# Performance work log

Measured on AMD Instinct MI355X. Metric: run time of the kernel, lower is better.

Reference implementation:

```python
import jax, jax.numpy as jnp
import numpy as np

N = 100000      # nodes
E = 1600000     # edges
IN_DIM = 128    # node_feat_dim
HID = 64        # hidden_dim
K = 3           # Chebyshev order
LAMBDA_MAX = 2.0  # PyG ChebConv default for 'sym' normalization


def setup_inputs():
    key = jax.random.key(0)
    ks = jax.random.split(key, 11)
    x = jax.random.normal(ks[0], (N, IN_DIM), jnp.float32)
    edge_index = jax.random.randint(ks[1], (2, E), 0, N)
    edge_weight = jax.random.uniform(ks[2], (E,), jnp.float32)
    h = jax.random.normal(ks[3], (N, HID), jnp.float32)
    c = jax.random.normal(ks[4], (N, HID), jnp.float32)
    s_in = 1.0 / np.sqrt(IN_DIM)
    s_h = 1.0 / np.sqrt(HID)
    # stacked gate params, order: [input, forget, cell(candidate), output]
    Wx = jax.random.uniform(ks[5], (4, IN_DIM, HID), jnp.float32, -s_in, s_in)
    bg = jax.random.uniform(ks[6], (4, HID), jnp.float32, -s_h, s_h)
    theta = jax.random.uniform(ks[7], (4, K, HID, HID), jnp.float32, -s_h, s_h)
    conv_b = jax.random.uniform(ks[8], (4, HID), jnp.float32, -s_h, s_h)
    Wl = jax.random.uniform(ks[9], (HID, HID), jnp.float32, -s_h, s_h)
    bl = jax.random.uniform(ks[10], (HID,), jnp.float32, -s_h, s_h)
    return dict(x=x, edge_index=edge_index, edge_weight=edge_weight, h=h, c=c,
                Wx=Wx, bg=bg, theta=theta, conv_b=conv_b, Wl=Wl, bl=bl)


def _make_lhat_mm(edge_index, edge_weight, num_nodes, lambda_max):
    # Builds z -> L_hat @ z  with  L_hat = (2/lambda_max) * (I - D^-1/2 A D^-1/2) - I
    src, dst = edge_index[0], edge_index[1]
    w = jnp.where(src == dst, 0.0, edge_weight)  # remove_self_loops
    deg = jax.ops.segment_sum(w, src, num_segments=num_nodes)
    deg_safe = jnp.where(deg > 0, deg, 1.0)
    dinv = jnp.where(deg > 0, jax.lax.rsqrt(deg_safe), 0.0)  # inf -> 0 as in PyG
    lap_w = (2.0 / lambda_max) * (-dinv[src] * w * dinv[dst])  # scaled off-diagonal
    diag = 2.0 / lambda_max - 1.0                              # scaled diag (0 at lmax=2)
    def lhat_mm(z):
        msg = lap_w[:, None] * z[src]                       # [E, HID] gather
        agg = jax.ops.segment_sum(msg, dst, num_segments=num_nodes)
        return agg + diag * z
    return lhat_mm


def reference(x, edge_index, edge_weight, h, c, Wx, bg, theta, conv_b, Wl, bl):
    lhat_mm = _make_lhat_mm(edge_index, edge_weight, x.shape[0], LAMBDA_MAX)
    # Chebyshev basis T_k(L_hat) h ; identical across the 4 gate ChebConvs, so compute once.
    Tx = [h, lhat_mm(h)]
    for _ in range(2, K):
        Tx.append(2.0 * lhat_mm(Tx[-1]) - Tx[-2])
    Tx = jnp.stack(Tx)                                      # [K, N, HID]
    conv = jnp.einsum('knh,gkho->gno', Tx, theta) + conv_b[:, None, :]
    lin = jnp.einsum('nf,gfo->gno', x, Wx) + bg[:, None, :]
    pre = lin + conv                                        # [4, N, HID]
    i = jax.nn.sigmoid(pre[0])
    f = jax.nn.sigmoid(pre[1])
    t = jnp.tanh(pre[2])
    o = jax.nn.sigmoid(pre[3])
    c0 = f * c + i * t
    h0 = o * jnp.tanh(c0)
    out = jax.nn.relu(h0) @ Wl + bl                         # trailing relu + Linear
    return (out, h0, c0)
```

## Files before the change

kernel.cpp:

```cpp
#include <hip/hip_runtime.h>
#include <hip/hip_bf16.h>

#define NN 100000
#define NE 1600000
#define INDIM 128
#define HID 64
#define BSH 9
#define NBUCK 196

typedef __hip_bfloat16 bf16;
typedef unsigned short ushort;
typedef unsigned int uint;
typedef __attribute__((ext_vector_type(8))) short short8;
typedef __attribute__((ext_vector_type(4))) float floatx4;

__device__ __forceinline__ float b2f(bf16 v) { return __bfloat162float(v); }
__device__ __forceinline__ float b2f_raw(ushort u) { return __uint_as_float(((uint)u) << 16); }
__device__ __forceinline__ ushort f2bu(float v) {
    bf16 t = __float2bfloat16(v);
    return *reinterpret_cast<ushort*>(&t);
}
__device__ __forceinline__ float ldin(const void* p, int i, int f32) {
    return f32 ? ((const float*)p)[i] : b2f(((const bf16*)p)[i]);
}
__device__ __forceinline__ float sigmoidf(float x) { return 1.f / (1.f + __expf(-x)); }
__device__ __forceinline__ float tanh_fast(float x) {
    float e = __expf(2.f * x);
    return 1.f - 2.f / (e + 1.f);
}
__device__ __forceinline__ uint4 packf8(const float* f) {
    uint4 u;
    u.x = f2bu(f[0]) | ((uint)f2bu(f[1]) << 16);
    u.y = f2bu(f[2]) | ((uint)f2bu(f[3]) << 16);
    u.z = f2bu(f[4]) | ((uint)f2bu(f[5]) << 16);
    u.w = f2bu(f[6]) | ((uint)f2bu(f[7]) << 16);
    return u;
}
__device__ __forceinline__ uint4 ld8_bf16(const void* p, int off, int f32) {
    if (!f32) return *(const uint4*)((const ushort*)p + off);
    const float* q = (const float*)p + off;
    float4 a = *(const float4*)q, b = *(const float4*)(q + 4);
    float f[8] = {a.x, a.y, a.z, a.w, b.x, b.y, b.z, b.w};
    return packf8(f);
}
__device__ __forceinline__ void ld4w(const void* ew, int e0, int f32, float* w) {
    if (f32) {
        float4 v = *(const float4*)((const float*)ew + e0);
        w[0] = v.x; w[1] = v.y; w[2] = v.z; w[3] = v.w;
    } else {
        uint2 v = *(const uint2*)((const ushort*)ew + e0);
        w[0] = b2f_raw((ushort)(v.x & 0xffff)); w[1] = b2f_raw((ushort)(v.x >> 16));
        w[2] = b2f_raw((ushort)(v.y & 0xffff)); w[3] = b2f_raw((ushort)(v.y >> 16));
    }
}

__global__ void k_sniff(const void* __restrict__ x, int* __restrict__ flag) {
    __shared__ int cnt;
    if (threadIdx.x == 0) cnt = 0;
    __syncthreads();
    const bf16* p = (const bf16*)x;
    int bad = 0;
    for (int i = threadIdx.x; i < 8192; i += 256) {
        float v = b2f(p[i]);
        if (!(fabsf(v) < 1e6f)) bad++;
    }
    atomicAdd(&cnt, bad);
    __syncthreads();
    if (threadIdx.x == 0) flag[0] = (cnt > 32) ? 1 : 0;
}

__global__ __launch_bounds__(256)
void k_count(const int* __restrict__ ei, int* __restrict__ gcntD,
             int* __restrict__ gcntS) {
    __shared__ int hD[NBUCK], hS[NBUCK];
    for (int i = threadIdx.x; i < NBUCK; i += 256) { hD[i] = 0; hS[i] = 0; }
    __syncthreads();
    int e0 = (blockIdx.x * 256 + threadIdx.x) * 16;
    if (e0 < NE) {
        if (e0 + 16 <= NE) {
#pragma unroll
            for (int q = 0; q < 4; q++) {
                int4 s4 = *(const int4*)(ei + e0 + q * 4);
                int4 d4 = *(const int4*)(ei + NE + e0 + q * 4);
                int ss[4] = {s4.x, s4.y, s4.z, s4.w};
                int dd[4] = {d4.x, d4.y, d4.z, d4.w};
#pragma unroll
                for (int j = 0; j < 4; j++)
                    if (ss[j] != dd[j]) {
                        atomicAdd(hD + (dd[j] >> BSH), 1);
                        atomicAdd(hS + (ss[j] >> BSH), 1);
                    }
            }
        } else {
            for (int e = e0; e < NE; e++) {
                int s = ei[e], d = ei[NE + e];
                if (s != d) {
                    atomicAdd(hD + (d >> BSH), 1);
                    atomicAdd(hS + (s >> BSH), 1);
                }
            }
        }
    }
    __syncthreads();
    for (int i = threadIdx.x; i < NBUCK; i += 256) {
        if (hD[i]) atomicAdd(gcntD + i, hD[i]);
        if (hS[i]) atomicAdd(gcntS + i, hS[i]);
    }
}

__global__ __launch_bounds__(256)
void k_scanb(const int* __restrict__ gcntD, const int* __restrict__ gcntS,
             int* __restrict__ bbaseD, int* __restrict__ bbaseS,
             int* __restrict__ gcurD, int* __restrict__ gcurS,
             int* __restrict__ rowptr) {
    __shared__ int sh[256];
    const int t = threadIdx.x;
    int v = (t < NBUCK) ? gcntD[t] : 0;
    sh[t] = v; __syncthreads();
    for (int off = 1; off < 256; off <<= 1) {
        int u = (t >= off) ? sh[t - off] : 0;
        __syncthreads(); sh[t] += u; __syncthreads();
    }
    if (t < NBUCK) { int e = sh[t] - v; bbaseD[t] = e; gcurD[t] = e; }
    if (t == 255) { bbaseD[NBUCK] = sh[255]; rowptr[NN] = sh[255]; }
    __syncthreads();
    int v2 = (t < NBUCK) ? gcntS[t] : 0;
    sh[t] = v2; __syncthreads();
    for (int off = 1; off < 256; off <<= 1) {
        int u = (t >= off) ? sh[t - off] : 0;
        __syncthreads(); sh[t] += u; __syncthreads();
    }
    if (t < NBUCK) { int e = sh[t] - v2; bbaseS[t] = e; gcurS[t] = e; }
    if (t == 255) bbaseS[NBUCK] = sh[255];
}

__global__ __launch_bounds__(256)
void k_part(const int* __restrict__ ei, const void* __restrict__ ew,
            int* __restrict__ gcurD, int* __restrict__ gcurS,
            int2* __restrict__ recD, int2* __restrict__ recS,
            const int* __restrict__ flagp) {
    const int f32 = flagp[0];
    __shared__ int cD[NBUCK], cS[NBUCK], bD[NBUCK], bS[NBUCK];
    for (int i = threadIdx.x; i < NBUCK; i += 256) { cD[i] = 0; cS[i] = 0; }
    __syncthreads();
    const int e0 = (blockIdx.x * 256 + threadIdx.x) * 8;
    int s[8], d[8], rD[8], rS[8];
    float w[8];
    bool act[8];
    if (e0 + 8 <= NE) {
        int4 sa = *(const int4*)(ei + e0), sb = *(const int4*)(ei + e0 + 4);
        int4 da = *(const int4*)(ei + NE + e0), db = *(const int4*)(ei + NE + e0 + 4);
        s[0]=sa.x; s[1]=sa.y; s[2]=sa.z; s[3]=sa.w;
        s[4]=sb.x; s[5]=sb.y; s[6]=sb.z; s[7]=sb.w;
        d[0]=da.x; d[1]=da.y; d[2]=da.z; d[3]=da.w;
        d[4]=db.x; d[5]=db.y; d[6]=db.z; d[7]=db.w;
        ld4w(ew, e0, f32, w); ld4w(ew, e0 + 4, f32, w + 4);
#pragma unroll
        for (int j = 0; j < 8; j++) act[j] = (s[j] != d[j]);
    } else {
#pragma unroll
        for (int j = 0; j < 8; j++) {
            int e = e0 + j;
            if (e < NE) {
                s[j] = ei[e]; d[j] = ei[NE + e]; w[j] = ldin(ew, e, f32);
                act[j] = (s[j] != d[j]);
            } else { s[j] = 0; d[j] = 0; w[j] = 0.f; act[j] = false; }
        }
    }
#pragma unroll
    for (int j = 0; j < 8; j++)
        if (act[j]) {
            rD[j] = atomicAdd(cD + (d[j] >> BSH), 1);
            rS[j] = atomicAdd(cS + (s[j] >> BSH), 1);
        }
    __syncthreads();
    for (int i = threadIdx.x; i < NBUCK; i += 256) {
        bD[i] = cD[i] ? atomicAdd(gcurD + i, cD[i]) : 0;
        bS[i] = cS[i] ? atomicAdd(gcurS + i, cS[i]) : 0;
    }
    __syncthreads();
#pragma unroll
    for (int j = 0; j < 8; j++)
        if (act[j]) {
            int2 pd; pd.x = s[j] | ((d[j] & 511) << 17); pd.y = __float_as_int(w[j]);
            recD[bD[d[j] >> BSH] + rD[j]] = pd;
            int2 ps; ps.x = s[j] & 511; ps.y = __float_as_int(w[j]);
            recS[bS[s[j] >> BSH] + rS[j]] = ps;
        }
}

__global__ __launch_bounds__(512)
void k_build(const int2* __restrict__ recD, const int2* __restrict__ recS,
             const int* __restrict__ bbaseD, const int* __restrict__ bbaseS,
             int* __restrict__ rowptr, int2* __restrict__ csr,
             float* __restrict__ dinv) {
    __shared__ int cnt[512], sh[512], cur[512];
    __shared__ float degf[512];
    const int t = threadIdx.x, b = blockIdx.x;
    cnt[t] = 0; degf[t] = 0.f;
    __syncthreads();
    const int dbase = bbaseD[b], dend = bbaseD[b + 1];
    const int sbase = bbaseS[b], send = bbaseS[b + 1];
    const int nD = dend - dbase, nS = send - sbase;
    const int2* rd = recD + dbase;
    const int2* rs = recS + sbase;
    for (int i = t; i < nD; i += 512) atomicAdd(cnt + (rd[i].x >> 17), 1);
    for (int i = t; i < nS; i += 512) atomicAdd(degf + rs[i].x, __int_as_float(rs[i].y));
    __syncthreads();
    const int own = cnt[t];
    sh[t] = own; __syncthreads();
    for (int off = 1; off < 512; off <<= 1) {
        int u = (t >= off) ? sh[t - off] : 0;
        __syncthreads(); sh[t] += u; __syncthreads();
    }
    const int rstart = dbase + sh[t] - own;
    cur[t] = rstart;
    const int node = (b << BSH) + t;
    if (node < NN) {
        rowptr[node] = rstart;
        float dg = degf[t];
        dinv[node] = dg > 0.f ? rsqrtf(dg) : 0.f;
    }
    __syncthreads();
    for (int i = t; i < nD; i += 512) {
        int2 r = rd[i];
        int pos = atomicAdd(cur + (r.x >> 17), 1);
        int2 o; o.x = r.x & 0x1FFFF; o.y = r.y;
        csr[pos] = o;
    }
}

template<int MODE>
__global__ __launch_bounds__(256)
void k_gath(const int* __restrict__ rowptr, const float* __restrict__ dinv,
            const int2* __restrict__ csr, const void* __restrict__ zin,
            const void* __restrict__ hin, ushort* __restrict__ outv,
            const int* __restrict__ flagp) {
    const int f32 = flagp[0];
    int n = (blockIdx.x * 256 + threadIdx.x) >> 6;
    int lane = threadIdx.x & 63;
    if (n >= NN) return;
    int b0 = rowptr[n], e0 = rowptr[n + 1];
    const int2* row = csr + b0;
    int cnt = e0 - b0;
    float acc = 0.f;
    int i = 0;
#define ZLD(sidx) (MODE == 0 ? ldin(zin, (sidx) * 64 + lane, f32) \
                             : b2f_raw(((const ushort*)zin)[(size_t)(sidx) * 128 + lane]))
    for (; i + 3 < cnt; i += 4) {
        int2 p0 = row[i], p1 = row[i + 1], p2 = row[i + 2], p3 = row[i + 3];
        float z0 = ZLD(p0.x), z1 = ZLD(p1.x), z2 = ZLD(p2.x), z3 = ZLD(p3.x);
        acc = fmaf(dinv[p0.x] * __int_as_float(p0.y), z0, acc);
        acc = fmaf(dinv[p1.x] * __int_as_float(p1.y), z1, acc);
        acc = fmaf(dinv[p2.x] * __int_as_float(p2.y), z2, acc);
        acc = fmaf(dinv[p3.x] * __int_as_float(p3.y), z3, acc);
    }
    for (; i < cnt; i++) {
        int2 p0 = row[i];
        float z0 = ZLD(p0.x);
        acc = fmaf(dinv[p0.x] * __int_as_float(p0.y), z0, acc);
    }
#undef ZLD
    float r = -dinv[n] * acc;
    if (MODE == 0) {
        outv[(size_t)n * 128 + lane] = f2bu(r);
    } else {
        float hv = ldin(hin, n * 64 + lane, f32);
        outv[(size_t)n * 128 + lane] = f2bu(2.f * r - hv);
    }
}

__global__ void k_wcat(const void* __restrict__ Wx, const void* __restrict__ theta,
                       const void* __restrict__ bg, const void* __restrict__ convb,
                       const void* __restrict__ Wl,
                       ushort* __restrict__ Wf, float* __restrict__ biasP,
                       ushort* __restrict__ WlF, const int* __restrict__ flagp) {
    const int f32 = flagp[0];
    int gid = blockIdx.x * 256 + threadIdx.x;
    if (gid < 81920) {
        int j = gid & 7, l = (gid >> 3) & 63, tile = gid >> 9;
        int kc = tile >> 4, t = tile & 15;
        int r = kc * 32 + ((l >> 4) * 8) + j;
        int g = t & 3;
        int cc = (t >> 2) * 16 + (l & 15);
        float v;
        if (r < 128) {
            v = ldin(Wx, (g * 128 + r) * 64 + cc, f32);
        } else {
            int k3 = (r - 128) >> 6, rr = (r - 128) & 63;
            v = ldin(theta, ((g * 3 + k3) * 64 + rr) * 64 + cc, f32);
        }
        Wf[gid] = f2bu(v);
        if (gid < 256) {
            int o = gid;
            int gg = (o >> 4) & 3;
            int cc2 = (o >> 6) * 16 + (o & 15);
            biasP[o] = ldin(bg, gg * 64 + cc2, f32) + ldin(convb, gg * 64 + cc2, f32);
        }
    } else {
        int gid2 = gid - 81920;
        int j = gid2 & 7, l = (gid2 >> 3) & 63, tile2 = gid2 >> 9;
        int kc2 = tile2 >> 2, t = tile2 & 3;
        int k = kc2 * 32 + ((l >> 4) * 8) + j;
        int n = t * 16 + (l & 15);
        WlF[gid2] = f2bu(ldin(Wl, k * 64 + n, f32));
    }
}

__global__ __launch_bounds__(256)
void k_gates(const void* __restrict__ x, const void* __restrict__ h,
             const void* __restrict__ cin,
             const ushort* __restrict__ Tx1, const ushort* __restrict__ Tx2,
             const ushort* __restrict__ Wf, const float* __restrict__ biasP,
             const ushort* __restrict__ WlF, const void* __restrict__ bl,
             float* __restrict__ outF, float* __restrict__ h0o,
             float* __restrict__ c0o, const int* __restrict__ flagp) {
    const int f32 = flagp[0];
    __shared__ ushort Hs[64 * 72];
    const int tid = threadIdx.x;
    const int lane = tid & 63;
    const int w = tid >> 6;
    const int base = blockIdx.x * 64;
    const int rown = lane & 15;
    const int kq = lane >> 4;

    floatx4 acc[4][4];
    {
        float bv0 = biasP[w * 64 + 0 * 16 + (lane & 15)];
        float bv1 = biasP[w * 64 + 1 * 16 + (lane & 15)];
        float bv2 = biasP[w * 64 + 2 * 16 + (lane & 15)];
        float bv3 = biasP[w * 64 + 3 * 16 + (lane & 15)];
#pragma unroll
        for (int mt = 0; mt < 4; mt++) {
            acc[mt][0] = (floatx4){bv0, bv0, bv0, bv0};
            acc[mt][1] = (floatx4){bv1, bv1, bv1, bv1};
            acc[mt][2] = (floatx4){bv2, bv2, bv2, bv2};
            acc[mt][3] = (floatx4){bv3, bv3, bv3, bv3};
        }
    }

    auto lda = [&](int mt, int kc) -> short8 {
        int node = base + mt * 16 + rown;
        uint4 r = {0, 0, 0, 0};
        if (node < NN) {
            if (kc < 4)      r = ld8_bf16(x, node * 128 + kc * 32 + kq * 8, f32);
            else if (kc < 6) r = ld8_bf16(h, node * 64 + (kc - 4) * 32 + kq * 8, f32);
            else if (kc < 8) r = *(const uint4*)&Tx1[(size_t)node * 128 + (kc - 6) * 32 + kq * 8];
            else             r = *(const uint4*)&Tx2[(size_t)node * 128 + (kc - 8) * 32 + kq * 8];
        }
        return *(short8*)&r;
    };

#pragma unroll
    for (int kc = 0; kc < 10; kc++) {
        short8 aF[4];
#pragma unroll
        for (int mt = 0; mt < 4; mt++) aF[mt] = lda(mt, kc);
        short8 bF[4];
#pragma unroll
        for (int g = 0; g < 4; g++)
            bF[g] = *(const short8*)&Wf[((kc * 16 + w * 4 + g) * 64 + lane) * 8];
#pragma unroll
        for (int mt = 0; mt < 4; mt++)
#pragma unroll
            for (int g = 0; g < 4; g++)
                acc[mt][g] = __builtin_amdgcn_mfma_f32_16x16x32_bf16(
                    aF[mt], bF[g], acc[mt][g], 0, 0, 0);
    }

    __syncthreads();

    const int cc = w * 16 + (lane & 15);
#pragma unroll
    for (int mt = 0; mt < 4; mt++) {
        const int m0 = mt * 16 + ((lane >> 4) * 4);
#pragma unroll
        for (int r = 0; r < 4; r++) {
            int ml = m0 + r;
            int node = base + ml;
            float gi = sigmoidf(acc[mt][0][r]);
            float gf = sigmoidf(acc[mt][1][r]);
            float gt = tanh_fast(acc[mt][2][r]);
            float go = sigmoidf(acc[mt][3][r]);
            float cv = (node < NN) ? ldin(cin, node * 64 + cc, f32) : 0.f;
            float c0 = gf * cv + gi * gt;
            float h0v = go * tanh_fast(c0);
            if (node < NN) {
                c0o[node * 64 + cc] = c0;
                h0o[node * 64 + cc] = h0v;
            }
            Hs[ml * 72 + cc] = f2bu(fmaxf(h0v, 0.f));
        }
    }
    __syncthreads();

    float blv = ldin(bl, w * 16 + (lane & 15), f32);
    floatx4 oacc[4];
#pragma unroll
    for (int mt = 0; mt < 4; mt++) oacc[mt] = (floatx4){blv, blv, blv, blv};
#pragma unroll
    for (int kc2 = 0; kc2 < 2; kc2++) {
        short8 bW = *(const short8*)&WlF[((kc2 * 4 + w) * 64 + lane) * 8];
#pragma unroll
        for (int mt = 0; mt < 4; mt++) {
            short8 aH = *(const short8*)&Hs[(mt * 16 + (lane & 15)) * 72
                                            + kc2 * 32 + (lane >> 4) * 8];
            oacc[mt] = __builtin_amdgcn_mfma_f32_16x16x32_bf16(
                aH, bW, oacc[mt], 0, 0, 0);
        }
    }
#pragma unroll
    for (int mt = 0; mt < 4; mt++) {
        const int m0 = mt * 16 + ((lane >> 4) * 4);
#pragma unroll
        for (int r = 0; r < 4; r++) {
            int node = base + m0 + r;
            if (node < NN)
                outF[node * 64 + w * 16 + (lane & 15)] = oacc[mt][r];
        }
    }
}

extern "C" void kernel_launch(void* const* d_in, const int* in_sizes, int n_in,
                              void* d_out, int out_size, void* d_ws, size_t ws_size,
                              hipStream_t stream) {
    const void* x     = d_in[0];
    const int*  ei    = (const int*)d_in[1];
    const void* ew    = d_in[2];
    const void* h     = d_in[3];
    const void* c     = d_in[4];
    const void* Wx    = d_in[5];
    const void* bg    = d_in[6];
    const void* theta = d_in[7];
    const void* convb = d_in[8];
    const void* Wl    = d_in[9];
    const void* bl    = d_in[10];
    (void)in_sizes; (void)n_in; (void)out_size; (void)ws_size;

    float*  ws     = (float*)d_ws;
    int*    flag   = (int*)ws;
    float*  dinv   = ws + 64;
    int*    rowptr = (int*)(ws + 100064);
    int*    gcntD  = (int*)(ws + 200128);
    int*    gcntS  = (int*)(ws + 200384);
    int*    bbaseD = (int*)(ws + 200640);
    int*    bbaseS = (int*)(ws + 200896);
    int*    gcurD  = (int*)(ws + 201152);
    int*    gcurS  = (int*)(ws + 201408);
    float*  biasP  = ws + 400128;
    ushort* Wf     = (ushort*)(ws + 400384);
    ushort* WlF    = (ushort*)(ws + 441344);

    float* outF = (float*)d_out;
    float* h0o  = outF + (size_t)NN * 64;
    float* c0o  = outF + (size_t)2 * NN * 64;
    ushort* Tx1b = (ushort*)outF;
    ushort* Tx2b = (ushort*)c0o;
    int2* recD = (int2*)h0o;
    int2* csr  = (int2*)(h0o + 3200000);
    int2* recS = (int2*)c0o;

    k_sniff<<<1, 256, 0, stream>>>(x, flag);
    hipMemsetAsync(gcntD, 0, 512 * 4, stream);

    k_count<<<(NE + 4095) / 4096, 256, 0, stream>>>(ei, gcntD, gcntS);
    k_scanb<<<1, 256, 0, stream>>>(gcntD, gcntS, bbaseD, bbaseS, gcurD, gcurS, rowptr);
    k_part<<<(NE + 2047) / 2048, 256, 0, stream>>>(ei, ew, gcurD, gcurS,
                                                   recD, recS, flag);
    k_build<<<NBUCK, 512, 0, stream>>>(recD, recS, bbaseD, bbaseS,
                                       rowptr, csr, dinv);
    k_wcat<<<336, 256, 0, stream>>>(Wx, theta, bg, convb, Wl, Wf, biasP, WlF, flag);

    k_gath<0><<<25000, 256, 0, stream>>>(rowptr, dinv, csr, h,    h, Tx1b, flag);
    k_gath<1><<<25000, 256, 0, stream>>>(rowptr, dinv, csr, Tx1b, h, Tx2b, flag);

    k_gates<<<(NN + 63) / 64, 256, 0, stream>>>(x, h, c, Tx1b, Tx2b,
                                                Wf, biasP, WlF, bl,
                                                outF, h0o, c0o, flag);
}
```

Before: 511.9 us.

## Stage gate A-tiles in LDS via direct global loads; cooperative edge fetch in gather

The gates kernel now loads the whole 64-node A tile (x, h, Tx1, Tx2) once into shared memory. In the bf16 path it uses global_load_lds, so each wave no longer re-fetches all four row tiles from global memory; the MFMA loop then reads its fragments from LDS. The gather kernel now loads up to 64 CSR entries per wave at once, one per lane, computes the edge weights lane-parallel, and broadcasts them with shuffles. This replaces each lane redundantly loading every edge record and its dinv value. The cost is an 40KB LDS allocation, which may lower occupancy, plus the added shuffle overhead.

```diff
diff --git a/kernel.cpp b/kernel.cpp
--- a/kernel.cpp
+++ b/kernel.cpp
@@ -52,6 +52,11 @@
         w[0] = b2f_raw((ushort)(v.x & 0xffff)); w[1] = b2f_raw((ushort)(v.x >> 16));
         w[2] = b2f_raw((ushort)(v.y & 0xffff)); w[3] = b2f_raw((ushort)(v.y >> 16));
     }
+}
+__device__ __forceinline__ void gl_lds16(const void* g, void* l) {
+    __builtin_amdgcn_global_load_lds(
+        (const __attribute__((address_space(1))) unsigned int*)g,
+        (__attribute__((address_space(3))) unsigned int*)l, 16, 0, 0);
 }
 
 __global__ void k_sniff(const void* __restrict__ x, int* __restrict__ flag) {
@@ -240,25 +245,31 @@
     int n = (blockIdx.x * 256 + threadIdx.x) >> 6;
     int lane = threadIdx.x & 63;
     if (n >= NN) return;
-    int b0 = rowptr[n], e0 = rowptr[n + 1];
+    int b0 = rowptr[n], e0r = rowptr[n + 1];
+    int cnt = e0r - b0;
     const int2* row = csr + b0;
-    int cnt = e0 - b0;
     float acc = 0.f;
-    int i = 0;
 #define ZLD(sidx) (MODE == 0 ? ldin(zin, (sidx) * 64 + lane, f32) \
                              : b2f_raw(((const ushort*)zin)[(size_t)(sidx) * 128 + lane]))
-    for (; i + 3 < cnt; i += 4) {
-        int2 p0 = row[i], p1 = row[i + 1], p2 = row[i + 2], p3 = row[i + 3];
-        float z0 = ZLD(p0.x), z1 = ZLD(p1.x), z2 = ZLD(p2.x), z3 = ZLD(p3.x);
-        acc = fmaf(dinv[p0.x] * __int_as_float(p0.y), z0, acc);
-        acc = fmaf(dinv[p1.x] * __int_as_float(p1.y), z1, acc);
-        acc = fmaf(dinv[p2.x] * __int_as_float(p2.y), z2, acc);
-        acc = fmaf(dinv[p3.x] * __int_as_float(p3.y), z3, acc);
-    }
-    for (; i < cnt; i++) {
-        int2 p0 = row[i];
-        float z0 = ZLD(p0.x);
-        acc = fmaf(dinv[p0.x] * __int_as_float(p0.y), z0, acc);
+    for (int ib = 0; ib < cnt; ib += 64) {
+        int idx = ib + lane;
+        int2 p;
+        if (idx < cnt) p = row[idx];
+        else { p.x = 0; p.y = 0; }
+        float sw = dinv[p.x] * __int_as_float(p.y);
+        int m = cnt - ib; if (m > 64) m = 64;
+        int m4 = (m + 3) & ~3;
+        for (int e = 0; e < m4; e += 4) {
+            int   s0 = __shfl(p.x, e),     s1 = __shfl(p.x, e + 1);
+            int   s2 = __shfl(p.x, e + 2), s3 = __shfl(p.x, e + 3);
+            float w0 = __shfl(sw, e),      w1 = __shfl(sw, e + 1);
+            float w2 = __shfl(sw, e + 2),  w3 = __shfl(sw, e + 3);
+            float z0 = ZLD(s0), z1 = ZLD(s1), z2 = ZLD(s2), z3 = ZLD(s3);
+            acc = fmaf(w0, z0, acc);
+            acc = fmaf(w1, z1, acc);
+            acc = fmaf(w2, z2, acc);
+            acc = fmaf(w3, z3, acc);
+        }
     }
 #undef ZLD
     float r = -dinv[n] * acc;
@@ -316,13 +327,41 @@
              float* __restrict__ outF, float* __restrict__ h0o,
              float* __restrict__ c0o, const int* __restrict__ flagp) {
     const int f32 = flagp[0];
-    __shared__ ushort Hs[64 * 72];
+    __shared__ ushort As[10 * 256 * 8];
     const int tid = threadIdx.x;
     const int lane = tid & 63;
     const int w = tid >> 6;
     const int base = blockIdx.x * 64;
-    const int rown = lane & 15;
-    const int kq = lane >> 4;
+
+    const int nodeS = base + ((tid >> 6) << 4) + (tid & 15);
+    const int kq8 = ((tid >> 4) & 3) * 8;
+    const bool okS = nodeS < NN;
+
+    if (!f32) {
+        if (okS) {
+#pragma unroll
+            for (int kc = 0; kc < 10; kc++) {
+                const ushort* g;
+                if (kc < 4)      g = (const ushort*)x + (size_t)nodeS * 128 + kc * 32 + kq8;
+                else if (kc < 6) g = (const ushort*)h + (size_t)nodeS * 64 + (kc - 4) * 32 + kq8;
+                else if (kc < 8) g = Tx1 + (size_t)nodeS * 128 + (kc - 6) * 32 + kq8;
+                else             g = Tx2 + (size_t)nodeS * 128 + (kc - 8) * 32 + kq8;
+                gl_lds16(g, &As[(kc * 256 + tid) * 8]);
+            }
+        }
+    } else {
+#pragma unroll
+        for (int kc = 0; kc < 10; kc++) {
+            uint4 raw = {0, 0, 0, 0};
+            if (okS) {
+                if (kc < 4)      raw = ld8_bf16(x, nodeS * 128 + kc * 32 + kq8, 1);
+                else if (kc < 6) raw = ld8_bf16(h, nodeS * 64 + (kc - 4) * 32 + kq8, 1);
+                else if (kc < 8) raw = *(const uint4*)&Tx1[(size_t)nodeS * 128 + (kc - 6) * 32 + kq8];
+                else             raw = *(const uint4*)&Tx2[(size_t)nodeS * 128 + (kc - 8) * 32 + kq8];
+            }
+            *(uint4*)&As[(kc * 256 + tid) * 8] = raw;
+        }
+    }
 
     floatx4 acc[4][4];
     {
@@ -339,23 +378,14 @@
         }
     }
 
-    auto lda = [&](int mt, int kc) -> short8 {
-        int node = base + mt * 16 + rown;
-        uint4 r = {0, 0, 0, 0};
-        if (node < NN) {
-            if (kc < 4)      r = ld8_bf16(x, node * 128 + kc * 32 + kq * 8, f32);
-            else if (kc < 6) r = ld8_bf16(h, node * 64 + (kc - 4) * 32 + kq * 8, f32);
-            else if (kc < 8) r = *(const uint4*)&Tx1[(size_t)node * 128 + (kc - 6) * 32 + kq * 8];
-            else             r = *(const uint4*)&Tx2[(size_t)node * 128 + (kc - 8) * 32 + kq * 8];
-        }
-        return *(short8*)&r;
-    };
+    __syncthreads();
 
 #pragma unroll
     for (int kc = 0; kc < 10; kc++) {
         short8 aF[4];
 #pragma unroll
-        for (int mt = 0; mt < 4; mt++) aF[mt] = lda(mt, kc);
+        for (int mt = 0; mt < 4; mt++)
+            aF[mt] = *(const short8*)&As[(kc * 256 + mt * 64 + lane) * 8];
         short8 bF[4];
 #pragma unroll
         for (int g = 0; g < 4; g++)
@@ -369,6 +399,8 @@
     }
 
     __syncthreads();
+
+    ushort* Hs = As;
 
     const int cc = w * 16 + (lane & 15);
 #pragma unroll
```

Result: faster. 426.7 us (-16.6%).
